# Optimization experiments

Hardware: AMD Instinct MI355X
Metric: run time of the kernel (lower is better)

## Reference

```python
import jax, jax.numpy as jnp
import numpy as np

K = 20
NEG = jnp.float32(-1e30)

def _l2norm(x):
    # F.normalize(x, dim=1, p=2) with eps clamp
    n = jnp.sqrt(jnp.sum(x * x, axis=1, keepdims=True))
    return x / jnp.maximum(n, 1e-12)

def setup_inputs() -> dict:
    key = jax.random.key(0)
    k1, k2, k3 = jax.random.split(key, 3)
    h, w, C = 96, 96, 256
    query_label = jax.random.randint(k1, (h, w, 3), 0, 2, dtype=jnp.int64)
    color = jnp.zeros((3,), dtype=jnp.int64)
    q_feat = jax.random.normal(k2, (1, C, h, w), dtype=jnp.float32)
    s_feat = jax.random.normal(k3, (1, C, h, w), dtype=jnp.float32)
    return {"query_label": query_label, "color": color, "q_feat": q_feat, "s_feat": s_feat}

def reference(query_label, color, q_feat, s_feat):
    C = q_feat.shape[1]
    out_hw = s_feat.shape[2:]
    # mask at feature resolution (query_label already sized [h,w,3])
    mask = jnp.all(query_label == color, axis=-1).reshape(-1)      # [M]
    q = q_feat[0].transpose(1, 2, 0).reshape(-1, C)                # [M,C]
    s = s_feat[0].transpose(1, 2, 0).reshape(-1, C)                # [N,C]
    qn = _l2norm(q)
    sn = _l2norm(s)
    sim = sn @ qn.T                                                # [N,M] cosine sims
    # top-K over fg columns == top-K over full row with non-fg masked to -inf
    fg_top = jax.lax.top_k(jnp.where(mask[None, :], sim, NEG), K)[0]
    bg_top = jax.lax.top_k(jnp.where(mask[None, :], NEG, sim), K)[0]
    fg_score = jnp.mean(fg_top, axis=1).reshape(out_hw)
    bg_score = jnp.mean(bg_top, axis=1).reshape(out_hw)
    return fg_score, bg_score
```

## Files before the change

### kernel.cpp

```cpp
#include <hip/hip_runtime.h>
#include <math.h>

#define MTOT 9216
#define CDIM 256
#define KSEL 20
#define NCHUNK 4
#define CHUNKQ 2304
#define BS 32
#define QSTEP 128
#define NSTEP 18
#define NSLAB 72

typedef __attribute__((ext_vector_type(8))) short short8;
typedef __attribute__((ext_vector_type(8))) unsigned short ushort8;
typedef __attribute__((ext_vector_type(4))) float f32x4;
typedef __attribute__((ext_vector_type(2))) _Float16 h2;

__device__ __forceinline__ unsigned short f2bf(float v) {
    unsigned u = __float_as_uint(v);
    u += 0x7FFF + ((u >> 16) & 1);
    return (unsigned short)(u >> 16);
}
__device__ __forceinline__ h2 pkh2(float lo, float hi) {
    auto r = __builtin_amdgcn_cvt_pkrtz(lo, hi);
    h2 h; __builtin_memcpy(&h, &r, 4); return h;
}
__device__ __forceinline__ h2 asH2(unsigned int u) {
    h2 h; __builtin_memcpy(&h, &u, 4); return h;
}
__device__ __forceinline__ unsigned int h2u(h2 h) {
    unsigned int u; __builtin_memcpy(&u, &h, 4); return u;
}
__device__ __forceinline__ h2 h2max(h2 a, h2 b) { return __builtin_elementwise_max(a, b); }
__device__ __forceinline__ h2 h2min(h2 a, h2 b) { return __builtin_elementwise_min(a, b); }
__device__ __forceinline__ unsigned short hbits(_Float16 x) {
    unsigned short u; __builtin_memcpy(&u, &x, 2); return u;
}
__device__ __forceinline__ float hs2f(unsigned short u) {
    _Float16 x; __builtin_memcpy(&x, &u, 2); return (float)x;
}

__device__ __forceinline__ void ins20p(h2 (&l)[KSEL], h2 v) {
    v = h2max(v, l[0]);
#pragma unroll
    for (int i = 0; i < KSEL - 1; ++i) {
        h2 nxt = l[i + 1];
        l[i] = h2min(nxt, v);
        v = h2max(nxt, v);
    }
    l[KSEL - 1] = v;
}
__device__ __forceinline__ void ins20(float (&l)[KSEL], float v) {
#pragma unroll
    for (int i = 0; i < KSEL - 1; ++i) {
        float nxt = l[i + 1];
        l[i] = fminf(nxt, v);
        v = fmaxf(nxt, v);
    }
    l[KSEL - 1] = v;
}

__global__ __launch_bounds__(256) void prepconv_kernel(
    const int* __restrict__ ql, const int* __restrict__ color,
    const float* __restrict__ qf, const float* __restrict__ sf,
    int* __restrict__ cnt,
    unsigned short* __restrict__ qbt, unsigned short* __restrict__ sbt)
{
    __shared__ float tilef[32 * 257];
    __shared__ float red[256];
    __shared__ float invv[32];
    __shared__ int slotl[32];
    const int bid = blockIdx.x;
    const bool isQ = bid < (MTOT / 32);
    const int m0 = (isQ ? bid : bid - MTOT / 32) * 32;
    const float* src = isQ ? qf : sf;
    const int t = threadIdx.x;
    const int ml = t & 31, cb = t >> 5;
    float sq = 0.f;
#pragma unroll
    for (int i = 0; i < 32; ++i) {
        int c = cb * 32 + i;
        float v = src[c * MTOT + m0 + ml];
        tilef[ml * 257 + c] = v;
        sq += v * v;
    }
    red[cb * 32 + ml] = sq;
    __syncthreads();
    if (t < 32) {
        float s = 0.f;
#pragma unroll
        for (int j = 0; j < 8; ++j) s += red[j * 32 + t];
        invv[t] = 1.0f / fmaxf(sqrtf(s), 1e-12f);
        if (isQ) {
            int m = m0 + t;
            bool fg = (ql[3*m] == color[0]) & (ql[3*m+1] == color[1]) & (ql[3*m+2] == color[2]);
            slotl[t] = fg ? atomicAdd(&cnt[0], 1) : (MTOT - 1 - atomicAdd(&cnt[1], 1));
        }
    }
    __syncthreads();
    const int row = t >> 3, seg = t & 7;
    const float iv = invv[row];
    const int drow = isQ ? slotl[row] : (m0 + row);
    unsigned short* dst = (isQ ? qbt : sbt) + (size_t)drow * 256 + seg * 32;
    const float* srcr = &tilef[row * 257 + seg * 32];
#pragma unroll
    for (int ch = 0; ch < 4; ++ch) {
        ushort8 o;
#pragma unroll
        for (int e = 0; e < 8; ++e) o[e] = f2bf(srcr[ch * 8 + e] * iv);
        *(ushort8*)(dst + ch * 8) = o;
    }
}

__global__ __launch_bounds__(256, 3) void matchsim_kernel(
    const unsigned short* __restrict__ qbt, const unsigned short* __restrict__ sbt,
    const int* __restrict__ cnt, unsigned short* __restrict__ part)
{
    __shared__ __align__(16) char smem[49152];
    unsigned int* mbuf = (unsigned int*)smem;

    const int t = threadIdx.x;
    const int w = t >> 6, l = t & 63;
    const int sblk = blockIdx.x >> 2;
    const int chunk = blockIdx.x & 3;
    const int s0 = sblk * BS;
    const int q0c = chunk * CHUNKQ;
    const int fgc = cnt[0];

    {
        int row = t >> 3, cb = t & 7;
        const ushort8* gs = (const ushort8*)(sbt + (size_t)(s0 + row) * 256);
#pragma unroll
        for (int i = 0; i < 4; ++i) {
            int ch = cb + i * 8;
            ushort8 v = gs[ch];
            int byte = (row * 512 + ch * 16) ^ ((row & 7) << 4);
            *(ushort8*)(smem + byte) = v;
        }
    }
    __syncthreads();

    const h2 NEG2 = { (_Float16)-65504.f, (_Float16)-65504.f };
    h2 fgl[KSEL], bgl[KSEL];
#pragma unroll
    for (int i = 0; i < KSEL; ++i) { fgl[i] = NEG2; bgl[i] = NEG2; }

    ushort8 qr[4];
    const int wl = (t & 63) >> 1;
    const int qhalf = t & 1;
    auto loadQ = [&](int gslab) {
        int step = gslab >> 2, slab = gslab & 3;
        const unsigned short* base =
            qbt + (size_t)(q0c + step * QSTEP + w * 32 + wl) * 256 + slab * 64 + qhalf * 32;
#pragma unroll
        for (int i = 0; i < 4; ++i)
            qr[i] = *(const ushort8*)(base + i * 8);
    };
    loadQ(0);
    const int qwswz = (wl & 7) << 4;
    char* const qbase = smem + 16384 + w * 4096;

    const int lg = l >> 4;
    const int aq0 = l & 15;
    const int aq1 = aq0 + 16;
    const int aswz0 = (aq0 & 7) << 4, aswz1 = (aq1 & 7) << 4;
    const int srow0 = l & 15, srow1 = srow0 + 16;
    const int bswz0 = (srow0 & 7) << 4, bswz1 = (srow1 & 7) << 4;

    f32x4 acc00 = {0,0,0,0}, acc01 = {0,0,0,0}, acc10 = {0,0,0,0}, acc11 = {0,0,0,0};
    int cur = 0;

    for (int gslab = 0; gslab < NSLAB; ++gslab) {
        char* Qs = qbase + cur * 16384;
#pragma unroll
        for (int i = 0; i < 4; ++i) {
            int byte = (wl * 128 + qhalf * 64 + i * 16) ^ qwswz;
            *(ushort8*)(Qs + byte) = qr[i];
        }
        if (gslab + 1 < NSLAB) loadQ(gslab + 1);
        const int slab = gslab & 3;
        __builtin_amdgcn_s_setprio(1);
#pragma unroll
        for (int ks = 0; ks < 2; ++ks) {
            int ak = ks * 64 + lg * 16;
            short8 a0 = *(const short8*)(Qs + ((aq0 * 128 + ak) ^ aswz0));
            short8 a1 = *(const short8*)(Qs + ((aq1 * 128 + ak) ^ aswz1));
            int bk = slab * 128 + ks * 64 + lg * 16;
            short8 b0 = *(const short8*)(smem + ((srow0 * 512 + bk) ^ bswz0));
            short8 b1 = *(const short8*)(smem + ((srow1 * 512 + bk) ^ bswz1));
            acc00 = __builtin_amdgcn_mfma_f32_16x16x32_bf16(a0, b0, acc00, 0, 0, 0);
            acc01 = __builtin_amdgcn_mfma_f32_16x16x32_bf16(a0, b1, acc01, 0, 0, 0);
            acc10 = __builtin_amdgcn_mfma_f32_16x16x32_bf16(a1, b0, acc10, 0, 0, 0);
            acc11 = __builtin_amdgcn_mfma_f32_16x16x32_bf16(a1, b1, acc11, 0, 0, 0);
        }
        __builtin_amdgcn_s_setprio(0);
        cur ^= 1;
        if (slab == 3) {
            const int step = gslab >> 2;
            const int qw0 = q0c + step * QSTEP + w * 32;
#pragma unroll
            for (int qt = 0; qt < 2; ++qt) {
                const f32x4& aS0 = qt ? acc10 : acc00;
                const f32x4& aS1 = qt ? acc11 : acc01;
                int qfirst = qw0 + qt * 16;
                if (qfirst + 16 <= fgc) {
#pragma unroll
                    for (int r = 0; r < 4; ++r) ins20p(fgl, pkh2(aS0[r], aS1[r]));
                } else if (qfirst >= fgc) {
#pragma unroll
                    for (int r = 0; r < 4; ++r) ins20p(bgl, pkh2(aS0[r], aS1[r]));
                } else {
#pragma unroll
                    for (int r = 0; r < 4; ++r) {
                        h2 v = pkh2(aS0[r], aS1[r]);
                        bool m = (qfirst + lg * 4 + r) < fgc;
                        ins20p(fgl, m ? v : NEG2);
                        ins20p(bgl, m ? NEG2 : v);
                    }
                }
            }
            acc00 = (f32x4){0,0,0,0}; acc01 = (f32x4){0,0,0,0};
            acc10 = (f32x4){0,0,0,0}; acc11 = (f32x4){0,0,0,0};
        }
    }

    __syncthreads();
    const int sp = l & 15, owner = w * 4 + lg;
    auto midx = [](int cls, int own, int spi) { return ((cls * 16 + own) * 16 + spi) * 21; };
    {
        unsigned int* df = &mbuf[midx(0, owner, sp)];
        unsigned int* db = &mbuf[midx(1, owner, sp)];
#pragma unroll
        for (int k = 0; k < KSEL; ++k) { df[k] = h2u(fgl[k]); db[k] = h2u(bgl[k]); }
    }
    __syncthreads();
    auto mergeL = [&](unsigned int* A, const unsigned int* B) {
        h2 la[KSEL];
#pragma unroll
        for (int k = 0; k < KSEL; ++k) la[k] = asH2(A[k]);
        for (int j = KSEL - 1; j >= 0; --j) {
            h2 v = asH2(B[j]);
            if (!(v.x > la[0].x || v.y > la[0].y)) break;
            ins20p(la, v);
        }
#pragma unroll
        for (int k = 0; k < KSEL; ++k) A[k] = h2u(la[k]);
    };
    {
        int cls = t >> 7, u = t & 127, spi = u & 15, j = u >> 4;
        mergeL(&mbuf[midx(cls, j, spi)], &mbuf[midx(cls, j + 8, spi)]);
    }
    __syncthreads();
    if (t < 128) {
        int cls = t >> 6, u = t & 63, spi = u & 15, j = u >> 4;
        mergeL(&mbuf[midx(cls, j, spi)], &mbuf[midx(cls, j + 4, spi)]);
    }
    __syncthreads();
    if (t < 64) {
        int cls = t >> 5, u = t & 31, spi = u & 15, j = u >> 4;
        mergeL(&mbuf[midx(cls, j, spi)], &mbuf[midx(cls, j + 2, spi)]);
    }
    __syncthreads();
    if (t < 32) {
        int cls = t >> 4, spi = t & 15;
        unsigned int* A = &mbuf[midx(cls, 0, spi)];
        const unsigned int* B = &mbuf[midx(cls, 1, spi)];
        h2 la[KSEL];
#pragma unroll
        for (int k = 0; k < KSEL; ++k) la[k] = asH2(A[k]);
        for (int j = KSEL - 1; j >= 0; --j) {
            h2 v = asH2(B[j]);
            if (!(v.x > la[0].x || v.y > la[0].y)) break;
            ins20p(la, v);
        }
        unsigned short* d0 = &part[((size_t)(s0 + spi)      * NCHUNK + chunk) * (2*KSEL) + cls*KSEL];
        unsigned short* d1 = &part[((size_t)(s0 + 16 + spi) * NCHUNK + chunk) * (2*KSEL) + cls*KSEL];
#pragma unroll
        for (int k = 0; k < KSEL; ++k) {
            d0[k] = hbits(la[k].x);
            d1[k] = hbits(la[k].y);
        }
    }
}

__global__ __launch_bounds__(256) void finalize_kernel(
    const unsigned short* __restrict__ part, float* __restrict__ out)
{
    int n = blockIdx.x * 256 + threadIdx.x;
    if (n >= MTOT) return;
    const unsigned short* base = part + (size_t)n * NCHUNK * 2 * KSEL;
#pragma unroll
    for (int cls = 0; cls < 2; ++cls) {
        float la[KSEL];
        const unsigned short* c0p = base + cls * KSEL;
#pragma unroll
        for (int k = 0; k < KSEL; ++k) la[k] = hs2f(c0p[k]);
        for (int ch = 1; ch < NCHUNK; ++ch) {
            const unsigned short* sp = base + ch * 2 * KSEL + cls * KSEL;
            for (int j = KSEL - 1; j >= 0; --j) {
                float v = hs2f(sp[j]);
                if (v <= la[0]) break;
                ins20(la, v);
            }
        }
        float s = 0.f;
#pragma unroll
        for (int k = 0; k < KSEL; ++k) s += la[k];
        out[cls * MTOT + n] = s * (1.0f / KSEL);
    }
}

extern "C" void kernel_launch(void* const* d_in, const int* in_sizes, int n_in,
                              void* d_out, int out_size, void* d_ws, size_t ws_size,
                              hipStream_t stream) {
    const int*   ql    = (const int*)d_in[0];
    const int*   color = (const int*)d_in[1];
    const float* qf    = (const float*)d_in[2];
    const float* sf    = (const float*)d_in[3];
    float* out = (float*)d_out;

    int* cnt = (int*)d_ws;
    unsigned short* qbt = (unsigned short*)(cnt + 4);
    unsigned short* sbt = qbt + (size_t)MTOT * CDIM;
    unsigned short* part = sbt + (size_t)MTOT * CDIM;

    (void)hipMemsetAsync(cnt, 0, 16, stream);
    prepconv_kernel<<<2 * (MTOT / 32), 256, 0, stream>>>(ql, color, qf, sf, cnt, qbt, sbt);
    matchsim_kernel<<<(MTOT / BS) * NCHUNK, 256, 0, stream>>>(qbt, sbt, cnt, part);
    finalize_kernel<<<MTOT / 256, 256, 0, stream>>>(part, out);
}
```

Measured before the change: 193.9 us.

## Split queries into six chunks, single-buffer Q smem, merge classes sequentially

Splits the query dimension into 6 chunks instead of 4, giving more blocks with shorter loops. Shared memory drops from 48KB to 32KB by removing the Q double buffer and by merging fg and bg top-K lists one class at a time in a smaller buffer. This allows 4 blocks per CU instead of 3. The tradeoffs are more partial lists for finalize to merge and more barriers. Removing the double buffer without adding a barrier also risks a race when a wave overwrites Q while its own lanes may still be reading it.

Measured after the change: 538.0 us. 2.78x slower.

```diff
diff --git a/kernel.cpp b/kernel.cpp
--- a/kernel.cpp
+++ b/kernel.cpp
@@ -4,12 +4,12 @@
 #define MTOT 9216
 #define CDIM 256
 #define KSEL 20
-#define NCHUNK 4
-#define CHUNKQ 2304
+#define NCHUNK 6
+#define CHUNKQ 1536
 #define BS 32
 #define QSTEP 128
-#define NSTEP 18
-#define NSLAB 72
+#define NSTEP 12
+#define NSLAB 48
 
 typedef __attribute__((ext_vector_type(8))) short short8;
 typedef __attribute__((ext_vector_type(8))) unsigned short ushort8;
@@ -112,17 +112,17 @@
     }
 }
 
-__global__ __launch_bounds__(256, 3) void matchsim_kernel(
+__global__ __launch_bounds__(256, 4) void matchsim_kernel(
     const unsigned short* __restrict__ qbt, const unsigned short* __restrict__ sbt,
     const int* __restrict__ cnt, unsigned short* __restrict__ part)
 {
-    __shared__ __align__(16) char smem[49152];
+    __shared__ __align__(16) char smem[32768];
     unsigned int* mbuf = (unsigned int*)smem;
 
     const int t = threadIdx.x;
     const int w = t >> 6, l = t & 63;
-    const int sblk = blockIdx.x >> 2;
-    const int chunk = blockIdx.x & 3;
+    const int sblk = blockIdx.x / NCHUNK;
+    const int chunk = blockIdx.x - sblk * NCHUNK;
     const int s0 = sblk * BS;
     const int q0c = chunk * CHUNKQ;
     const int fgc = cnt[0];
@@ -158,7 +158,7 @@
     };
     loadQ(0);
     const int qwswz = (wl & 7) << 4;
-    char* const qbase = smem + 16384 + w * 4096;
+    char* const Qs = smem + 16384 + w * 4096;
 
     const int lg = l >> 4;
     const int aq0 = l & 15;
@@ -168,10 +168,8 @@
     const int bswz0 = (srow0 & 7) << 4, bswz1 = (srow1 & 7) << 4;
 
     f32x4 acc00 = {0,0,0,0}, acc01 = {0,0,0,0}, acc10 = {0,0,0,0}, acc11 = {0,0,0,0};
-    int cur = 0;
 
     for (int gslab = 0; gslab < NSLAB; ++gslab) {
-        char* Qs = qbase + cur * 16384;
 #pragma unroll
         for (int i = 0; i < 4; ++i) {
             int byte = (wl * 128 + qhalf * 64 + i * 16) ^ qwswz;
@@ -194,7 +192,6 @@
             acc11 = __builtin_amdgcn_mfma_f32_16x16x32_bf16(a1, b1, acc11, 0, 0, 0);
         }
         __builtin_amdgcn_s_setprio(0);
-        cur ^= 1;
         if (slab == 3) {
             const int step = gslab >> 2;
             const int qw0 = q0c + step * QSTEP + w * 32;
@@ -225,15 +222,8 @@
     }
 
     __syncthreads();
+
     const int sp = l & 15, owner = w * 4 + lg;
-    auto midx = [](int cls, int own, int spi) { return ((cls * 16 + own) * 16 + spi) * 21; };
-    {
-        unsigned int* df = &mbuf[midx(0, owner, sp)];
-        unsigned int* db = &mbuf[midx(1, owner, sp)];
-#pragma unroll
-        for (int k = 0; k < KSEL; ++k) { df[k] = h2u(fgl[k]); db[k] = h2u(bgl[k]); }
-    }
-    __syncthreads();
     auto mergeL = [&](unsigned int* A, const unsigned int* B) {
         h2 la[KSEL];
 #pragma unroll
@@ -246,40 +236,53 @@
 #pragma unroll
         for (int k = 0; k < KSEL; ++k) A[k] = h2u(la[k]);
     };
-    {
-        int cls = t >> 7, u = t & 127, spi = u & 15, j = u >> 4;
-        mergeL(&mbuf[midx(cls, j, spi)], &mbuf[midx(cls, j + 8, spi)]);
-    }
-    __syncthreads();
-    if (t < 128) {
-        int cls = t >> 6, u = t & 63, spi = u & 15, j = u >> 4;
-        mergeL(&mbuf[midx(cls, j, spi)], &mbuf[midx(cls, j + 4, spi)]);
-    }
-    __syncthreads();
-    if (t < 64) {
-        int cls = t >> 5, u = t & 31, spi = u & 15, j = u >> 4;
-        mergeL(&mbuf[midx(cls, j, spi)], &mbuf[midx(cls, j + 2, spi)]);
-    }
-    __syncthreads();
-    if (t < 32) {
-        int cls = t >> 4, spi = t & 15;
-        unsigned int* A = &mbuf[midx(cls, 0, spi)];
-        const unsigned int* B = &mbuf[midx(cls, 1, spi)];
-        h2 la[KSEL];
-#pragma unroll
-        for (int k = 0; k < KSEL; ++k) la[k] = asH2(A[k]);
-        for (int j = KSEL - 1; j >= 0; --j) {
-            h2 v = asH2(B[j]);
-            if (!(v.x > la[0].x || v.y > la[0].y)) break;
-            ins20p(la, v);
-        }
-        unsigned short* d0 = &part[((size_t)(s0 + spi)      * NCHUNK + chunk) * (2*KSEL) + cls*KSEL];
-        unsigned short* d1 = &part[((size_t)(s0 + 16 + spi) * NCHUNK + chunk) * (2*KSEL) + cls*KSEL];
-#pragma unroll
-        for (int k = 0; k < KSEL; ++k) {
-            d0[k] = hbits(la[k].x);
-            d1[k] = hbits(la[k].y);
-        }
+    auto midx = [](int own, int spi) { return (own * 16 + spi) * 21; };
+
+#pragma unroll
+    for (int cls = 0; cls < 2; ++cls) {
+        const h2 (&lst)[KSEL] = cls ? bgl : fgl;
+        {
+            unsigned int* d = &mbuf[midx(owner, sp)];
+#pragma unroll
+            for (int k = 0; k < KSEL; ++k) d[k] = h2u(lst[k]);
+        }
+        __syncthreads();
+        if (t < 128) {
+            int spi = t & 15, j = t >> 4;
+            mergeL(&mbuf[midx(j, spi)], &mbuf[midx(j + 8, spi)]);
+        }
+        __syncthreads();
+        if (t < 64) {
+            int spi = t & 15, j = t >> 4;
+            mergeL(&mbuf[midx(j, spi)], &mbuf[midx(j + 4, spi)]);
+        }
+        __syncthreads();
+        if (t < 32) {
+            int spi = t & 15, j = t >> 4;
+            mergeL(&mbuf[midx(j, spi)], &mbuf[midx(j + 2, spi)]);
+        }
+        __syncthreads();
+        if (t < 16) {
+            int spi = t;
+            unsigned int* A = &mbuf[midx(0, spi)];
+            const unsigned int* B = &mbuf[midx(1, spi)];
+            h2 la[KSEL];
+#pragma unroll
+            for (int k = 0; k < KSEL; ++k) la[k] = asH2(A[k]);
+            for (int j = KSEL - 1; j >= 0; --j) {
+                h2 v = asH2(B[j]);
+                if (!(v.x > la[0].x || v.y > la[0].y)) break;
+                ins20p(la, v);
+            }
+            unsigned short* d0 = &part[((size_t)(s0 + spi)      * NCHUNK + chunk) * (2*KSEL) + cls*KSEL];
+            unsigned short* d1 = &part[((size_t)(s0 + 16 + spi) * NCHUNK + chunk) * (2*KSEL) + cls*KSEL];
+#pragma unroll
+            for (int k = 0; k < KSEL; ++k) {
+                d0[k] = hbits(la[k].x);
+                d1[k] = hbits(la[k].y);
+            }
+        }
+        __syncthreads();
     }
 }
 
```
